# Kernel tuning notes

Hardware: AMD Instinct MI355X
Metric: run time of the kernel (lower is better)

Reference implementation:

```python
import jax, jax.numpy as jnp
import numpy as np

DIM = 192
HEADS = 6
EPS = 1e-12  # torch F.normalize eps


def setup_inputs() -> dict:
    key = jax.random.key(0)
    k1, k2, k3, k4 = jax.random.split(key, 4)
    x = jax.random.normal(k1, (8, DIM, 128, 128), dtype=jnp.float32)
    # qkv: Conv2d(dim, 3*dim, k=3, pad=1, bias=False) -> OIHW weight
    qkv_w = jax.random.normal(k2, (3 * DIM, DIM, 3, 3), dtype=jnp.float32) * (1.0 / np.sqrt(DIM * 9))
    # project_out: Conv2d(dim, dim, k=1, bias=True)
    proj_w = jax.random.normal(k3, (DIM, DIM, 1, 1), dtype=jnp.float32) * (1.0 / np.sqrt(DIM))
    proj_b = jax.random.normal(k4, (DIM,), dtype=jnp.float32) * 0.01
    temperature = jnp.ones((HEADS, 1, 1), dtype=jnp.float32)
    return {"x": x, "qkv_w": qkv_w, "proj_w": proj_w, "proj_b": proj_b, "temperature": temperature}


def _conv2d(x, w, padding):
    return jax.lax.conv_general_dilated(
        x, w, window_strides=(1, 1), padding=padding,
        dimension_numbers=("NCHW", "OIHW", "NCHW"))


def reference(x, qkv_w, proj_w, proj_b, temperature):
    n, c, h, w = x.shape
    ch = c // HEADS  # channels per head
    qkv = _conv2d(x, qkv_w, ((1, 1), (1, 1)))  # [n, 3c, h, w]
    q, k, v = jnp.split(qkv, 3, axis=1)
    # n (head c) h w -> n head c (h*w)
    def to_heads(t):
        return t.reshape(n, HEADS, ch, h * w)
    q, k, v = to_heads(q), to_heads(k), to_heads(v)
    # L2 normalize over HW (last dim)
    q = q / jnp.maximum(jnp.linalg.norm(q, axis=-1, keepdims=True), EPS)
    k = k / jnp.maximum(jnp.linalg.norm(k, axis=-1, keepdims=True), EPS)
    # channel-wise cosine attention: [n, head, c, c]
    attn = jnp.einsum("nhcp,nhdp->nhcd", q, k) * temperature
    attn = jax.nn.softmax(attn, axis=-1)
    out = jnp.einsum("nhcd,nhdp->nhcp", attn, v)  # [n, head, ch, hw]
    out = out.reshape(n, c, h, w)
    out = _conv2d(out, proj_w, ((0, 0), (0, 0))) + proj_b[None, :, None, None]
    return out
```

## Files before the change

### kernel.cpp

```cpp
#include <hip/hip_runtime.h>
#include <stdint.h>

#define DIM 192
#define HEADS 6
#define HW 16384
#define CO 576
#define K9 1728
#define CQK 384

typedef __attribute__((ext_vector_type(8))) short bf16x8;
typedef __attribute__((ext_vector_type(4))) float f32x4;

__device__ __forceinline__ unsigned short f2bf(float f) {
  union { float f; unsigned u; } v; v.f = f;
  unsigned r = v.u + 0x7FFFu + ((v.u >> 16) & 1u);
  return (unsigned short)(r >> 16);
}

__device__ __forceinline__ void gll16(const void* g, void* l) {
  __builtin_amdgcn_global_load_lds(
      (const __attribute__((address_space(1))) unsigned int*)g,
      (__attribute__((address_space(3))) unsigned int*)l, 16, 0, 0);
}

__global__ __launch_bounds__(256) void k_reorder_w(const float* __restrict__ w,
                                                   unsigned short* __restrict__ wbf) {
  int g = blockIdx.x * 256 + threadIdx.x;
  if (g >= CO * K9) return;
  int o = g / K9, rem = g % K9;
  int rs = rem / DIM, ci = rem % DIM;
  wbf[g] = f2bf(w[(o * DIM + ci) * 9 + rs]);
}

__global__ __launch_bounds__(256) void k_nhwc(const float* __restrict__ x,
                                              unsigned short* __restrict__ xbf) {
  int g = blockIdx.x * 256 + threadIdx.x;
  int xcol = g & 127;
  int t2 = g >> 7;
  int c24 = t2 % 24;
  int t3 = t2 / 24;
  int y = t3 & 127;
  int n = t3 >> 7;
  union { unsigned short u[8]; uint4 v; } pk;
#pragma unroll
  for (int i = 0; i < 8; ++i)
    pk.u[i] = f2bf(x[((size_t)(n * DIM + c24 * 8 + i) * 128 + y) * 128 + xcol]);
  *(uint4*)&xbf[(size_t)((n * 128 + y) * 128 + xcol) * DIM + c24 * 8] = pk.v;
}

__global__ __launch_bounds__(256) void k_conv(const unsigned short* __restrict__ xbf,
                                              const unsigned short* __restrict__ wbf,
                                              const char* __restrict__ zeros,
                                              unsigned short* __restrict__ qkv,
                                              unsigned short* __restrict__ vt) {
  __shared__ char smem[2 * 40960];
  const int tid = threadIdx.x;
  const int lane = tid & 63;
  const int wv = tid >> 6;
  const int lane15 = lane & 15;
  const int lgrp = lane >> 4;

  int p = blockIdx.x;
  int xcd = p & 7;
  int slot = p >> 3;
  int work = xcd * 576 + slot;
  int cblk = work % 9;
  int g = work / 9;
  const int by = g & 63;
  const int n = g >> 6;
  const int c0 = cblk * 64;
  const int y0 = by * 2;

  f32x4 acc[4][4] = {};

  auto stage = [&](int t, int buf) {
    int rs = t / 3;
    int ci0 = (t % 3) * 64;
    int r = rs / 3, s = rs % 3;
    char* base = smem + buf * 40960;
#pragma unroll
    for (int rr = 0; rr < 2; ++rr) {
      int off = tid * 16 + rr * 4096;
      int row = off >> 7;
      int scb = (off & 127) ^ ((row & 7) << 4);
      const char* gp = (const char*)wbf + (size_t)((c0 + row) * K9 + rs * DIM + ci0) * 2 + scb;
      gll16(gp, base + rr * 4096 + wv * 1024);
    }
    int yb = y0 + r - 1;
#pragma unroll
    for (int rr = 0; rr < 8; ++rr) {
      int off = tid * 16 + rr * 4096;
      int prow = off >> 7;
      int scb = (off & 127) ^ ((prow & 7) << 4);
      int yy = yb + (prow >> 7);
      int xx = (prow & 127) + s - 1;
      const char* gp;
      if (yy < 0 || yy > 127 || xx < 0 || xx > 127)
        gp = zeros + scb;
      else
        gp = (const char*)xbf + (size_t)(((n * 128 + yy) * 128 + xx) * DIM + ci0) * 2 + scb;
      gll16(gp, base + 8192 + rr * 4096 + wv * 1024);
    }
  };

  auto compute = [&](int buf) {
    char* Ab = smem + buf * 40960;
    char* Bb = Ab + 8192;
#pragma unroll
    for (int k32 = 0; k32 < 2; ++k32) {
      int kb = k32 * 64 + lgrp * 16;
      bf16x8 a[4], b[4];
#pragma unroll
      for (int m = 0; m < 4; ++m) {
        int row = m * 16 + lane15;
        a[m] = *(bf16x8*)(Ab + row * 128 + (kb ^ ((row & 7) << 4)));
      }
#pragma unroll
      for (int nb = 0; nb < 4; ++nb) {
        int pp = wv * 64 + nb * 16 + lane15;
        b[nb] = *(bf16x8*)(Bb + pp * 128 + (kb ^ ((pp & 7) << 4)));
      }
#pragma unroll
      for (int m = 0; m < 4; ++m)
#pragma unroll
        for (int nb = 0; nb < 4; ++nb)
          acc[m][nb] = __builtin_amdgcn_mfma_f32_16x16x32_bf16(a[m], b[nb], acc[m][nb], 0, 0, 0);
    }
  };

  stage(0, 0);
  __syncthreads();
  int cur = 0;
  for (int t = 0; t < 27; ++t) {
    if (t < 26) stage(t + 1, cur ^ 1);
    compute(cur);
    __syncthreads();
    cur ^= 1;
  }

  char* st = smem;
  if (cblk < 6) {
#pragma unroll
    for (int m = 0; m < 4; ++m)
#pragma unroll
      for (int nb = 0; nb < 4; ++nb) {
        int pix = wv * 64 + nb * 16 + lane15;
#pragma unroll
        for (int j = 0; j < 4; ++j) {
          int c = m * 16 + lgrp * 4 + j;
          *(unsigned short*)(st + c * 512 + ((pix * 2) ^ ((c & 7) << 4))) = f2bf(acc[m][nb][j]);
        }
      }
    __syncthreads();
    int c = tid >> 2, q4 = tid & 3;
    char* dst = (char*)qkv + ((size_t)(n * CQK + c0 + c) * HW + by * 256 + q4 * 64) * 2;
#pragma unroll
    for (int i = 0; i < 8; ++i) {
      uint4 vv = *(uint4*)(st + c * 512 + ((q4 * 128 + i * 16) ^ ((c & 7) << 4)));
      *(uint4*)(dst + i * 16) = vv;
    }
  } else {
    int dg0 = c0 - 384;
#pragma unroll
    for (int m = 0; m < 4; ++m)
#pragma unroll
      for (int nb = 0; nb < 4; ++nb) {
        int pix = wv * 64 + nb * 16 + lane15;
        int cl = m * 16 + lgrp * 4;
        union { unsigned short u[4]; uint2 v; } pk;
#pragma unroll
        for (int j = 0; j < 4; ++j) pk.u[j] = f2bf(acc[m][nb][j]);
        *(uint2*)(st + pix * 128 + ((cl * 2) ^ ((pix & 7) << 4))) = pk.v;
      }
    __syncthreads();
    char* dst = (char*)vt + ((size_t)(n * HW + by * 256 + tid) * DIM + dg0) * 2;
#pragma unroll
    for (int i = 0; i < 8; ++i) {
      uint4 vv = *(uint4*)(st + tid * 128 + ((i * 16) ^ ((tid & 7) << 4)));
      *(uint4*)(dst + i * 16) = vv;
    }
  }
}

__global__ __launch_bounds__(256) void k_gram(const unsigned short* __restrict__ qkv,
                                              float* __restrict__ G) {
  const int pc = blockIdx.x, h = blockIdx.y, n = blockIdx.z;
  const int tid = threadIdx.x, lane = tid & 63, wv = tid >> 6;
  const int lane15 = lane & 15, lgrp = lane >> 4;
  const unsigned short* base[4];
#pragma unroll
  for (int mi = 0; mi < 4; ++mi) {
    int ch = mi * 16 + lane15;
    int cg = (ch < 32) ? (h * 32 + ch) : (DIM + h * 32 + ch - 32);
    base[mi] = qkv + (size_t)(n * CQK + cg) * HW;
  }
  f32x4 acc[4][4] = {};
  int pbase = pc * 2048 + wv * 512;
  for (int st = 0; st < 16; ++st) {
    int p = pbase + st * 32 + lgrp * 8;
    bf16x8 f[4];
#pragma unroll
    for (int mi = 0; mi < 4; ++mi) f[mi] = *(const bf16x8*)(base[mi] + p);
#pragma unroll
    for (int mi = 0; mi < 4; ++mi)
#pragma unroll
      for (int ni = 0; ni < 4; ++ni)
        acc[mi][ni] = __builtin_amdgcn_mfma_f32_16x16x32_bf16(f[mi], f[ni], acc[mi][ni], 0, 0, 0);
  }
  float* Gm = G + (size_t)(n * HEADS + h) * 4096;
#pragma unroll
  for (int mi = 0; mi < 4; ++mi)
#pragma unroll
    for (int ni = 0; ni < 4; ++ni)
#pragma unroll
      for (int j = 0; j < 4; ++j) {
        int row = mi * 16 + lgrp * 4 + j;
        int col = ni * 16 + lane15;
        atomicAdd(&Gm[row * 64 + col], acc[mi][ni][j]);
      }
}

__global__ __launch_bounds__(256) void k_attnm(const float* __restrict__ G,
                                               const float* __restrict__ temp,
                                               const float* __restrict__ projw,
                                               unsigned short* __restrict__ Mbf) {
  __shared__ float attn_s[HEADS][32][32];
  int n = blockIdx.x, tid = threadIdx.x;
  if (tid < 192) {
    int h = tid >> 5, c = tid & 31;
    const float* Gm = G + (size_t)(n * HEADS + h) * 4096;
    float nq = fmaxf(sqrtf(Gm[c * 64 + c]), 1e-12f);
    float tp = temp[h];
    float l[32];
    float mx = -1e30f;
#pragma unroll
    for (int d = 0; d < 32; ++d) {
      float nk = fmaxf(sqrtf(Gm[(32 + d) * 64 + 32 + d]), 1e-12f);
      l[d] = Gm[c * 64 + 32 + d] / (nq * nk) * tp;
      mx = fmaxf(mx, l[d]);
    }
    float sum = 0.f;
#pragma unroll
    for (int d = 0; d < 32; ++d) { l[d] = expf(l[d] - mx); sum += l[d]; }
    float inv = 1.f / sum;
#pragma unroll
    for (int d = 0; d < 32; ++d) attn_s[h][c][d] = l[d] * inv;
  }
  __syncthreads();
  for (int idx = tid; idx < DIM * DIM; idx += 256) {
    int o = idx / DIM, dg = idx % DIM;
    int h = dg >> 5, d = dg & 31;
    float s = 0.f;
#pragma unroll
    for (int c = 0; c < 32; ++c)
      s += projw[o * DIM + h * 32 + c] * attn_s[h][c][d];
    Mbf[(size_t)(n * DIM + o) * DIM + dg] = f2bf(s);
  }
}

__global__ __launch_bounds__(256) void k_out(const unsigned short* __restrict__ Mbf,
                                             const unsigned short* __restrict__ vt,
                                             const float* __restrict__ bias,
                                             float* __restrict__ out) {
  __shared__ char smem[2 * 40960];
  const int tid = threadIdx.x;
  const int lane = tid & 63;
  const int wv = tid >> 6;
  const int lane15 = lane & 15;
  const int lgrp = lane >> 4;
  const int c0 = blockIdx.x * 64;
  const int p0 = blockIdx.y * 256;
  const int n = blockIdx.z;

  f32x4 acc[4][4] = {};

  auto stage = [&](int t, int buf) {
    char* base = smem + buf * 40960;
#pragma unroll
    for (int rr = 0; rr < 2; ++rr) {
      int off = tid * 16 + rr * 4096;
      int row = off >> 7;
      int scb = (off & 127) ^ ((row & 7) << 4);
      const char* gp = (const char*)Mbf + (size_t)(n * DIM + c0 + row) * 384 + t * 128 + scb;
      gll16(gp, base + rr * 4096 + wv * 1024);
    }
#pragma unroll
    for (int rr = 0; rr < 8; ++rr) {
      int off = tid * 16 + rr * 4096;
      int prow = off >> 7;
      int scb = (off & 127) ^ ((prow & 7) << 4);
      const char* gp = (const char*)vt + (size_t)(n * HW + p0 + prow) * 384 + t * 128 + scb;
      gll16(gp, base + 8192 + rr * 4096 + wv * 1024);
    }
  };

  auto compute = [&](int buf) {
    char* Ab = smem + buf * 40960;
    char* Bb = Ab + 8192;
#pragma unroll
    for (int k32 = 0; k32 < 2; ++k32) {
      int kb = k32 * 64 + lgrp * 16;
      bf16x8 a[4], b[4];
#pragma unroll
      for (int m = 0; m < 4; ++m) {
        int row = m * 16 + lane15;
        a[m] = *(bf16x8*)(Ab + row * 128 + (kb ^ ((row & 7) << 4)));
      }
#pragma unroll
      for (int nb = 0; nb < 4; ++nb) {
        int pp = wv * 64 + nb * 16 + lane15;
        b[nb] = *(bf16x8*)(Bb + pp * 128 + (kb ^ ((pp & 7) << 4)));
      }
#pragma unroll
      for (int m = 0; m < 4; ++m)
#pragma unroll
        for (int nb = 0; nb < 4; ++nb)
          acc[m][nb] = __builtin_amdgcn_mfma_f32_16x16x32_bf16(a[m], b[nb], acc[m][nb], 0, 0, 0);
    }
  };

  stage(0, 0);
  __syncthreads();
  int cur = 0;
  for (int t = 0; t < 3; ++t) {
    if (t < 2) stage(t + 1, cur ^ 1);
    compute(cur);
    __syncthreads();
    cur ^= 1;
  }

#pragma unroll
  for (int m = 0; m < 4; ++m)
#pragma unroll
    for (int nb = 0; nb < 4; ++nb)
#pragma unroll
      for (int j = 0; j < 4; ++j) {
        int c = c0 + m * 16 + lgrp * 4 + j;
        int pix = wv * 64 + nb * 16 + lane15;
        out[(size_t)(n * DIM + c) * HW + p0 + pix] = acc[m][nb][j] + bias[c];
      }
}

extern "C" void kernel_launch(void* const* d_in, const int* in_sizes, int n_in,
                              void* d_out, int out_size, void* d_ws, size_t ws_size,
                              hipStream_t stream) {
  const float* x      = (const float*)d_in[0];
  const float* qkv_w  = (const float*)d_in[1];
  const float* proj_w = (const float*)d_in[2];
  const float* proj_b = (const float*)d_in[3];
  const float* temp   = (const float*)d_in[4];
  float* out = (float*)d_out;

  char* ws = (char*)d_ws;
  float* G            = (float*)ws;
  const char* zeros   = ws + 786432;
  unsigned short* wbf = (unsigned short*)(ws + 786688);
  unsigned short* qkv = (unsigned short*)(ws + 2777344);
  unsigned short* Mbf = (unsigned short*)(ws + 103440640);
  unsigned short* xbf = (unsigned short*)(ws + 104030464);
  unsigned short* vt  = (unsigned short*)(ws + 154362112);

  (void)hipMemsetAsync(ws, 0, 786688, stream);
  k_reorder_w<<<(CO * K9 + 255) / 256, 256, 0, stream>>>(qkv_w, wbf);
  k_nhwc<<<12288, 256, 0, stream>>>(x, xbf);
  k_conv<<<4608, 256, 0, stream>>>(xbf, wbf, zeros, qkv, vt);
  k_gram<<<dim3(8, HEADS, 8), 256, 0, stream>>>(qkv, G);
  k_attnm<<<8, 256, 0, stream>>>(G, temp, proj_w, Mbf);
  k_out<<<dim3(3, 64, 8), 256, 0, stream>>>(Mbf, vt, proj_b, out);
}
```

Before: 757.7 us.

## Drop LDS double buffering in conv and output GEMMs to raise occupancy

Both the 3x3 conv GEMM and the output projection GEMM now use a single 40 KB LDS buffer instead of two, and declare launch bounds of 4 blocks per CU. The intent is to fit more resident blocks per CU so that other blocks can hide global-load latency, in place of in-block prefetch of the next K slice. In exchange, each block now serializes load, barrier, compute, barrier with no overlap of its own, and the register cap may cause spills.

```diff
diff --git a/kernel.cpp b/kernel.cpp
--- a/kernel.cpp
+++ b/kernel.cpp
@@ -48,12 +48,12 @@
   *(uint4*)&xbf[(size_t)((n * 128 + y) * 128 + xcol) * DIM + c24 * 8] = pk.v;
 }
 
-__global__ __launch_bounds__(256) void k_conv(const unsigned short* __restrict__ xbf,
-                                              const unsigned short* __restrict__ wbf,
-                                              const char* __restrict__ zeros,
-                                              unsigned short* __restrict__ qkv,
-                                              unsigned short* __restrict__ vt) {
-  __shared__ char smem[2 * 40960];
+__global__ __launch_bounds__(256, 4) void k_conv(const unsigned short* __restrict__ xbf,
+                                                 const unsigned short* __restrict__ wbf,
+                                                 const char* __restrict__ zeros,
+                                                 unsigned short* __restrict__ qkv,
+                                                 unsigned short* __restrict__ vt) {
+  __shared__ char smem[40960];
   const int tid = threadIdx.x;
   const int lane = tid & 63;
   const int wv = tid >> 6;
@@ -73,18 +73,17 @@
 
   f32x4 acc[4][4] = {};
 
-  auto stage = [&](int t, int buf) {
+  auto stage = [&](int t) {
     int rs = t / 3;
     int ci0 = (t % 3) * 64;
     int r = rs / 3, s = rs % 3;
-    char* base = smem + buf * 40960;
 #pragma unroll
     for (int rr = 0; rr < 2; ++rr) {
       int off = tid * 16 + rr * 4096;
       int row = off >> 7;
       int scb = (off & 127) ^ ((row & 7) << 4);
       const char* gp = (const char*)wbf + (size_t)((c0 + row) * K9 + rs * DIM + ci0) * 2 + scb;
-      gll16(gp, base + rr * 4096 + wv * 1024);
+      gll16(gp, smem + rr * 4096 + wv * 1024);
     }
     int yb = y0 + r - 1;
 #pragma unroll
@@ -99,13 +98,13 @@
         gp = zeros + scb;
       else
         gp = (const char*)xbf + (size_t)(((n * 128 + yy) * 128 + xx) * DIM + ci0) * 2 + scb;
-      gll16(gp, base + 8192 + rr * 4096 + wv * 1024);
+      gll16(gp, smem + 8192 + rr * 4096 + wv * 1024);
     }
   };
 
-  auto compute = [&](int buf) {
-    char* Ab = smem + buf * 40960;
-    char* Bb = Ab + 8192;
+  auto compute = [&]() {
+    char* Ab = smem;
+    char* Bb = smem + 8192;
 #pragma unroll
     for (int k32 = 0; k32 < 2; ++k32) {
       int kb = k32 * 64 + lgrp * 16;
@@ -128,14 +127,11 @@
     }
   };
 
-  stage(0, 0);
-  __syncthreads();
-  int cur = 0;
   for (int t = 0; t < 27; ++t) {
-    if (t < 26) stage(t + 1, cur ^ 1);
-    compute(cur);
-    __syncthreads();
-    cur ^= 1;
+    stage(t);
+    __syncthreads();
+    compute();
+    __syncthreads();
   }
 
   char* st = smem;
@@ -258,11 +254,11 @@
   }
 }
 
-__global__ __launch_bounds__(256) void k_out(const unsigned short* __restrict__ Mbf,
-                                             const unsigned short* __restrict__ vt,
-                                             const float* __restrict__ bias,
-                                             float* __restrict__ out) {
-  __shared__ char smem[2 * 40960];
+__global__ __launch_bounds__(256, 4) void k_out(const unsigned short* __restrict__ Mbf,
+                                                const unsigned short* __restrict__ vt,
+                                                const float* __restrict__ bias,
+                                                float* __restrict__ out) {
+  __shared__ char smem[40960];
   const int tid = threadIdx.x;
   const int lane = tid & 63;
   const int wv = tid >> 6;
@@ -274,15 +270,14 @@
 
   f32x4 acc[4][4] = {};
 
-  auto stage = [&](int t, int buf) {
-    char* base = smem + buf * 40960;
+  auto stage = [&](int t) {
 #pragma unroll
     for (int rr = 0; rr < 2; ++rr) {
       int off = tid * 16 + rr * 4096;
       int row = off >> 7;
       int scb = (off & 127) ^ ((row & 7) << 4);
       const char* gp = (const char*)Mbf + (size_t)(n * DIM + c0 + row) * 384 + t * 128 + scb;
-      gll16(gp, base + rr * 4096 + wv * 1024);
+      gll16(gp, smem + rr * 4096 + wv * 1024);
     }
 #pragma unroll
     for (int rr = 0; rr < 8; ++rr) {
@@ -290,13 +285,13 @@
       int prow = off >> 7;
       int scb = (off & 127) ^ ((prow & 7) << 4);
       const char* gp = (const char*)vt + (size_t)(n * HW + p0 + prow) * 384 + t * 128 + scb;
-      gll16(gp, base + 8192 + rr * 4096 + wv * 1024);
+      gll16(gp, smem + 8192 + rr * 4096 + wv * 1024);
     }
   };
 
-  auto compute = [&](int buf) {
-    char* Ab = smem + buf * 40960;
-    char* Bb = Ab + 8192;
+  auto compute = [&]() {
+    char* Ab = smem;
+    char* Bb = smem + 8192;
 #pragma unroll
     for (int k32 = 0; k32 < 2; ++k32) {
       int kb = k32 * 64 + lgrp * 16;
@@ -319,14 +314,11 @@
     }
   };
 
-  stage(0, 0);
-  __syncthreads();
-  int cur = 0;
   for (int t = 0; t < 3; ++t) {
-    if (t < 2) stage(t + 1, cur ^ 1);
-    compute(cur);
-    __syncthreads();
-    cur ^= 1;
+    stage(t);
+    __syncthreads();
+    compute();
+    __syncthreads();
   }
 
 #pragma unroll
```

Result: faster. 644.6 us (-14.9%).
